# Optimization experiments

Measured on AMD Instinct MI355X. Metric: run time of the kernel, lower is better.

The kernel has to match this reference:

```python
import jax, jax.numpy as jnp
import numpy as np

IMG_C = 256
GC = 32  # graph_channel; must equal graph feature dim 32 for the residual


def setup_inputs() -> dict:
    key = jax.random.key(0)
    ks = jax.random.split(key, 10)
    B, N, WH_SIDE = 8, 4096, 64
    s = lambda fan_in: 1.0 / np.sqrt(fan_in)
    return {
        "input_graph": jax.random.normal(ks[0], (B, N, GC), jnp.float32),
        "input_image": jax.random.normal(ks[1], (B, IMG_C, WH_SIDE, WH_SIDE), jnp.float32),
        # Conv1d(kernel=1) weights stored as [out, in]
        "Wq": jax.random.uniform(ks[2], (GC, 32), jnp.float32, -s(32), s(32)),
        "bq": jax.random.uniform(ks[3], (GC,), jnp.float32, -s(32), s(32)),
        "Wk": jax.random.uniform(ks[4], (GC, IMG_C), jnp.float32, -s(IMG_C), s(IMG_C)),
        "bk": jax.random.uniform(ks[5], (GC,), jnp.float32, -s(IMG_C), s(IMG_C)),
        "Wv": jax.random.uniform(ks[6], (GC, IMG_C), jnp.float32, -s(IMG_C), s(IMG_C)),
        "bv": jax.random.uniform(ks[7], (GC,), jnp.float32, -s(IMG_C), s(IMG_C)),
        "Wc": jax.random.uniform(ks[8], (GC, GC), jnp.float32, -s(GC), s(GC)),
        "bc": jax.random.uniform(ks[9], (GC,), jnp.float32, -s(GC), s(GC)),
    }


def reference(input_graph, input_image, Wq, bq, Wk, bk, Wv, bv, Wc, bc):
    B, C, W, H = input_image.shape
    img = input_image.reshape(B, C, W * H)                      # [B, C, L]
    # 1x1 conv projections == channel matmuls
    K = jnp.einsum('oc,bcl->bol', Wk, img) + bk[None, :, None]  # [B, GC, L]
    V = jnp.einsum('oc,bcl->bol', Wv, img) + bv[None, :, None]  # [B, GC, L]
    # Q: graph [B, N, 32] -> conv over channel dim -> [B, N, GC]
    Q = jnp.einsum('oc,bnc->bno', Wq, input_graph) + bq[None, None, :]
    att = jnp.einsum('bno,bol->bnl', Q, K) / jnp.sqrt(jnp.float32(GC))  # [B, N, L]
    # NOTE: original softmax is over dim=1 (the node/query axis)
    att = jax.nn.softmax(att, axis=1)
    message = jnp.einsum('bol,bnl->bon', V, att)                # [B, GC, N]
    out = input_graph.transpose(0, 2, 1) + (
        jnp.einsum('oc,bcn->bon', Wc, message) + bc[None, :, None]
    )                                                           # [B, GC, N]
    return out.transpose(0, 2, 1)                               # [B, N, GC]
```

## Files before the change

kernel.cpp:

```cpp
#include <hip/hip_runtime.h>

#define BB 8
#define NN 4096
#define LL 4096
#define CC 256

typedef short bf16x8 __attribute__((ext_vector_type(8)));
typedef _Float16 f16x8 __attribute__((ext_vector_type(8)));
typedef _Float16 f16x2 __attribute__((ext_vector_type(2)));
typedef __fp16 hf16x2 __attribute__((ext_vector_type(2)));
typedef float f32x4 __attribute__((ext_vector_type(4)));

__device__ __forceinline__ short f2bf(float f) {
  union { float f; unsigned u; } v; v.f = f;
  unsigned r = v.u + 0x7fffu + ((v.u >> 16) & 1u);
  return (short)(r >> 16);
}
__device__ __forceinline__ bf16x8 ld8(const float* __restrict__ fp) {
  float4 a = *(const float4*)fp;
  float4 b = *(const float4*)(fp + 4);
  bf16x8 r;
  r[0] = f2bf(a.x); r[1] = f2bf(a.y); r[2] = f2bf(a.z); r[3] = f2bf(a.w);
  r[4] = f2bf(b.x); r[5] = f2bf(b.y); r[6] = f2bf(b.z); r[7] = f2bf(b.w);
  return r;
}

__global__ __launch_bounds__(256) void ka_proj(
    const float* __restrict__ graph, const float* __restrict__ img,
    const float* __restrict__ Wq, const float* __restrict__ bq,
    const float* __restrict__ Wk, const float* __restrict__ bk,
    const float* __restrict__ Wv, const float* __restrict__ bv,
    short* __restrict__ Qb, short* __restrict__ Kt, _Float16* __restrict__ Vt)
{
  const int tid = threadIdx.x;
  const int w = tid >> 6, lane = tid & 63, lo = lane & 15, q = lane >> 4;
  const int bid = blockIdx.x;
  if (bid < 512) {
    const int b = bid >> 6;
    const int lt = ((bid & 63) << 6) + (w << 4);
    f32x4 aK0 = {0,0,0,0}, aK1 = {0,0,0,0}, aV0 = {0,0,0,0}, aV1 = {0,0,0,0};
    const float* ib = img + (size_t)b * CC * LL + lt + lo;
    #pragma unroll
    for (int cs = 0; cs < 8; ++cs) {
      const int c0 = cs * 32 + q * 8;
      bf16x8 bi;
      #pragma unroll
      for (int j = 0; j < 8; ++j) bi[j] = f2bf(ib[(size_t)(c0 + j) * LL]);
      bf16x8 wk0 = ld8(Wk + lo * CC + c0);
      bf16x8 wk1 = ld8(Wk + (lo + 16) * CC + c0);
      bf16x8 wv0 = ld8(Wv + lo * CC + c0);
      bf16x8 wv1 = ld8(Wv + (lo + 16) * CC + c0);
      aK0 = __builtin_amdgcn_mfma_f32_16x16x32_bf16(wk0, bi, aK0, 0, 0, 0);
      aK1 = __builtin_amdgcn_mfma_f32_16x16x32_bf16(wk1, bi, aK1, 0, 0, 0);
      aV0 = __builtin_amdgcn_mfma_f32_16x16x32_bf16(wv0, bi, aV0, 0, 0, 0);
      aV1 = __builtin_amdgcn_mfma_f32_16x16x32_bf16(wv1, bi, aV1, 0, 0, 0);
    }
    const float kscale = 0.2550348663f;
    const size_t row = ((size_t)b * LL + lt + lo) * 32;
    short4 s0, s1;
    s0.x = f2bf((aK0[0] + bk[q * 4 + 0]) * kscale);
    s0.y = f2bf((aK0[1] + bk[q * 4 + 1]) * kscale);
    s0.z = f2bf((aK0[2] + bk[q * 4 + 2]) * kscale);
    s0.w = f2bf((aK0[3] + bk[q * 4 + 3]) * kscale);
    s1.x = f2bf((aK1[0] + bk[16 + q * 4 + 0]) * kscale);
    s1.y = f2bf((aK1[1] + bk[16 + q * 4 + 1]) * kscale);
    s1.z = f2bf((aK1[2] + bk[16 + q * 4 + 2]) * kscale);
    s1.w = f2bf((aK1[3] + bk[16 + q * 4 + 3]) * kscale);
    *(short4*)(Kt + row + q * 4) = s0;
    *(short4*)(Kt + row + 16 + q * 4) = s1;
    union { hf16x2 h[2]; uint2 u; } p0, p1;
    p0.h[0] = __builtin_amdgcn_cvt_pkrtz(aV0[0] + bv[q * 4 + 0], aV0[1] + bv[q * 4 + 1]);
    p0.h[1] = __builtin_amdgcn_cvt_pkrtz(aV0[2] + bv[q * 4 + 2], aV0[3] + bv[q * 4 + 3]);
    p1.h[0] = __builtin_amdgcn_cvt_pkrtz(aV1[0] + bv[16 + q * 4 + 0], aV1[1] + bv[16 + q * 4 + 1]);
    p1.h[1] = __builtin_amdgcn_cvt_pkrtz(aV1[2] + bv[16 + q * 4 + 2], aV1[3] + bv[16 + q * 4 + 3]);
    *(uint2*)(Vt + row + q * 4) = p0.u;
    *(uint2*)(Vt + row + 16 + q * 4) = p1.u;
  } else {
    const int t = bid - 512;
    const int b = t >> 6;
    const int nt = ((t & 63) << 6) + (w << 4);
    bf16x8 ag = ld8(graph + ((size_t)b * NN + nt + lo) * 32 + q * 8);
    bf16x8 w0 = ld8(Wq + lo * 32 + q * 8);
    bf16x8 w1 = ld8(Wq + (lo + 16) * 32 + q * 8);
    f32x4 z = {0,0,0,0};
    f32x4 a0 = __builtin_amdgcn_mfma_f32_16x16x32_bf16(ag, w0, z, 0, 0, 0);
    f32x4 a1 = __builtin_amdgcn_mfma_f32_16x16x32_bf16(ag, w1, z, 0, 0, 0);
    const float b0 = bq[lo], b1 = bq[lo + 16];
    #pragma unroll
    for (int r = 0; r < 4; ++r) {
      const size_t rowq = ((size_t)b * NN + nt + q * 4 + r) * 32;
      Qb[rowq + lo] = f2bf(a0[r] + b0);
      Qb[rowq + 16 + lo] = f2bf(a1[r] + b1);
    }
  }
}

__global__ __launch_bounds__(1024) void kb_z(
    const short* __restrict__ Qb, const short* __restrict__ Kt,
    const _Float16* __restrict__ Vt, _Float16* __restrict__ Vpp)
{
  __shared__ float zpart[16][64];
  __shared__ float zinv[64];
  const int tid = threadIdx.x;
  const int w = tid >> 6, lane = tid & 63, lo = lane & 15, q = lane >> 4;
  const int b = blockIdx.x >> 6;
  const int l0 = (blockIdx.x & 63) << 6;
  bf16x8 kf[4];
  #pragma unroll
  for (int f = 0; f < 4; ++f)
    kf[f] = *(const bf16x8*)(Kt + ((size_t)b * LL + l0 + f * 16 + lo) * 32 + q * 8);
  float za[4][4] = {{0}};
  const short* qbase = Qb + ((size_t)b * NN + w * 256 + lo) * 32 + q * 8;
  for (int it = 0; it < 16; ++it) {
    bf16x8 qf = *(const bf16x8*)(qbase + it * 512);
    #pragma unroll
    for (int f = 0; f < 4; ++f) {
      f32x4 z = {0,0,0,0};
      f32x4 c = __builtin_amdgcn_mfma_f32_16x16x32_bf16(kf[f], qf, z, 0, 0, 0);
      #pragma unroll
      for (int r = 0; r < 4; ++r) za[f][r] += __builtin_amdgcn_exp2f(c[r]);
    }
  }
  #pragma unroll
  for (int m = 1; m < 16; m <<= 1)
    #pragma unroll
    for (int f = 0; f < 4; ++f)
      #pragma unroll
      for (int r = 0; r < 4; ++r)
        za[f][r] += __shfl_xor(za[f][r], m, 64);
  if (lo == 0) {
    #pragma unroll
    for (int f = 0; f < 4; ++f)
      #pragma unroll
      for (int r = 0; r < 4; ++r)
        zpart[w][f * 16 + q * 4 + r] = za[f][r];
  }
  __syncthreads();
  if (tid < 64) {
    float z = 0.f;
    #pragma unroll
    for (int t = 0; t < 16; ++t) z += zpart[t][tid];
    zinv[tid] = 4096.0f / z;
  }
  __syncthreads();
  {
    const int l = tid & 63, og = tid >> 6;
    const float inv = zinv[l];
    const f16x2 vv = *(const f16x2*)(Vt + ((size_t)b * LL + l0 + l) * 32 + og * 2);
    Vpp[((size_t)b * 32 + og * 2 + 0) * LL + l0 + l] = (_Float16)((float)vv[0] * inv);
    Vpp[((size_t)b * 32 + og * 2 + 1) * LL + l0 + l] = (_Float16)((float)vv[1] * inv);
  }
}

__global__ __launch_bounds__(256) void kc_attn(
    const short* __restrict__ Qb, const short* __restrict__ Kt,
    const _Float16* __restrict__ Vpp, const float* __restrict__ graph,
    const float* __restrict__ Wc, const float* __restrict__ bc,
    float* __restrict__ out)
{
  __shared__ __align__(16) _Float16 P[4][32][72];
  __shared__ __align__(16) float msgL[4][32][36];
  const int tid = threadIdx.x;
  const int w = tid >> 6, lane = tid & 63, lo = lane & 15, q = lane >> 4;
  const int b = blockIdx.x >> 7;
  const int n0 = (blockIdx.x & 127) << 5;
  const bf16x8 qf0 = *(const bf16x8*)(Qb + ((size_t)b * NN + n0 + lo) * 32 + q * 8);
  const bf16x8 qf1 = *(const bf16x8*)(Qb + ((size_t)b * NN + n0 + 16 + lo) * 32 + q * 8);
  f32x4 m00 = {0,0,0,0}, m01 = {0,0,0,0}, m10 = {0,0,0,0}, m11 = {0,0,0,0};
  const short* ktb = Kt + (size_t)b * LL * 32 + lo * 32 + q * 8;
  const _Float16* vb0 = Vpp + ((size_t)b * 32 + lo) * LL;
  const _Float16* vb1 = vb0 + (size_t)16 * LL;
  for (int lc = w * 16; lc < w * 16 + 16; ++lc) {
    const int lbase = lc * 64;
    #pragma unroll
    for (int f = 0; f < 4; ++f) {
      bf16x8 kf = *(const bf16x8*)(ktb + (size_t)(lbase + f * 16) * 32);
      f32x4 z = {0,0,0,0};
      f32x4 c0 = __builtin_amdgcn_mfma_f32_16x16x32_bf16(kf, qf0, z, 0, 0, 0);
      f32x4 c1 = __builtin_amdgcn_mfma_f32_16x16x32_bf16(kf, qf1, z, 0, 0, 0);
      union { hf16x2 h[2]; uint2 u; } pk0, pk1;
      pk0.h[0] = __builtin_amdgcn_cvt_pkrtz(__builtin_amdgcn_exp2f(c0[0]),
                                            __builtin_amdgcn_exp2f(c0[1]));
      pk0.h[1] = __builtin_amdgcn_cvt_pkrtz(__builtin_amdgcn_exp2f(c0[2]),
                                            __builtin_amdgcn_exp2f(c0[3]));
      pk1.h[0] = __builtin_amdgcn_cvt_pkrtz(__builtin_amdgcn_exp2f(c1[0]),
                                            __builtin_amdgcn_exp2f(c1[1]));
      pk1.h[1] = __builtin_amdgcn_cvt_pkrtz(__builtin_amdgcn_exp2f(c1[2]),
                                            __builtin_amdgcn_exp2f(c1[3]));
      *(uint2*)&P[w][lo][f * 16 + q * 4] = pk0.u;
      *(uint2*)&P[w][16 + lo][f * 16 + q * 4] = pk1.u;
    }
    #pragma unroll
    for (int k = 0; k < 2; ++k) {
      f16x8 pa0 = *(const f16x8*)&P[w][lo][k * 32 + q * 8];
      f16x8 pa1 = *(const f16x8*)&P[w][16 + lo][k * 32 + q * 8];
      f16x8 v0 = *(const f16x8*)(vb0 + lbase + k * 32 + q * 8);
      f16x8 v1 = *(const f16x8*)(vb1 + lbase + k * 32 + q * 8);
      m00 = __builtin_amdgcn_mfma_f32_16x16x32_f16(pa0, v0, m00, 0, 0, 0);
      m01 = __builtin_amdgcn_mfma_f32_16x16x32_f16(pa0, v1, m01, 0, 0, 0);
      m10 = __builtin_amdgcn_mfma_f32_16x16x32_f16(pa1, v0, m10, 0, 0, 0);
      m11 = __builtin_amdgcn_mfma_f32_16x16x32_f16(pa1, v1, m11, 0, 0, 0);
    }
  }
  #pragma unroll
  for (int r = 0; r < 4; ++r) {
    msgL[w][q * 4 + r][lo] = m00[r];
    msgL[w][q * 4 + r][16 + lo] = m01[r];
    msgL[w][16 + q * 4 + r][lo] = m10[r];
    msgL[w][16 + q * 4 + r][16 + lo] = m11[r];
  }
  __syncthreads();
  const int o = lane & 31, nh = lane >> 5;
  float wcr[32];
  #pragma unroll
  for (int c4 = 0; c4 < 8; ++c4) {
    float4 wc4 = *(const float4*)(Wc + o * 32 + c4 * 4);
    wcr[c4 * 4 + 0] = wc4.x * (1.0f / 4096.0f);
    wcr[c4 * 4 + 1] = wc4.y * (1.0f / 4096.0f);
    wcr[c4 * 4 + 2] = wc4.z * (1.0f / 4096.0f);
    wcr[c4 * 4 + 3] = wc4.w * (1.0f / 4096.0f);
  }
  const float bcv = bc[o];
  #pragma unroll
  for (int rr = 0; rr < 4; ++rr) {
    const int nl = w * 8 + nh * 4 + rr;
    f32x4 s = {0,0,0,0};
    #pragma unroll
    for (int cc = 0; cc < 8; ++cc) {
      f32x4 ma = *(const f32x4*)&msgL[0][nl][cc * 4];
      f32x4 mb = *(const f32x4*)&msgL[1][nl][cc * 4];
      f32x4 mc = *(const f32x4*)&msgL[2][nl][cc * 4];
      f32x4 md = *(const f32x4*)&msgL[3][nl][cc * 4];
      f32x4 m4 = ma + mb + mc + md;
      s[0] += wcr[cc * 4 + 0] * m4[0];
      s[1] += wcr[cc * 4 + 1] * m4[1];
      s[2] += wcr[cc * 4 + 2] * m4[2];
      s[3] += wcr[cc * 4 + 3] * m4[3];
    }
    const size_t idx = ((size_t)b * NN + n0 + nl) * 32 + o;
    out[idx] = s[0] + s[1] + s[2] + s[3] + bcv + graph[idx];
  }
}

extern "C" void kernel_launch(void* const* d_in, const int* in_sizes, int n_in,
                              void* d_out, int out_size, void* d_ws, size_t ws_size,
                              hipStream_t stream) {
  const float* graph = (const float*)d_in[0];
  const float* img   = (const float*)d_in[1];
  const float* Wq    = (const float*)d_in[2];
  const float* bq    = (const float*)d_in[3];
  const float* Wk    = (const float*)d_in[4];
  const float* bk    = (const float*)d_in[5];
  const float* Wv    = (const float*)d_in[6];
  const float* bv    = (const float*)d_in[7];
  const float* Wc    = (const float*)d_in[8];
  const float* bc    = (const float*)d_in[9];
  char* ws = (char*)d_ws;
  short*    Qb  = (short*)(ws + 0);
  short*    Kt  = (short*)(ws + 2097152);
  _Float16* Vt  = (_Float16*)(ws + 4194304);
  _Float16* Vpp = (_Float16*)(ws + 6291456);
  ka_proj<<<dim3(1024), dim3(256), 0, stream>>>(graph, img, Wq, bq, Wk, bk, Wv, bv,
                                                Qb, Kt, Vt);
  kb_z<<<dim3(512), dim3(1024), 0, stream>>>(Qb, Kt, Vt, Vpp);
  kc_attn<<<dim3(1024), dim3(256), 0, stream>>>(Qb, Kt, Vpp, graph, Wc, bc,
                                                (float*)d_out);
}
```

Before: 209.2 us.

## Split column-normalizer into atomic partial-sum pass, add K/V prefetch in attention

```diff
diff --git a/kernel.cpp b/kernel.cpp
--- a/kernel.cpp
+++ b/kernel.cpp
@@ -7,7 +7,6 @@
 
 typedef short bf16x8 __attribute__((ext_vector_type(8)));
 typedef _Float16 f16x8 __attribute__((ext_vector_type(8)));
-typedef _Float16 f16x2 __attribute__((ext_vector_type(2)));
 typedef __fp16 hf16x2 __attribute__((ext_vector_type(2)));
 typedef float f32x4 __attribute__((ext_vector_type(4)));
 
@@ -30,13 +29,15 @@
     const float* __restrict__ Wq, const float* __restrict__ bq,
     const float* __restrict__ Wk, const float* __restrict__ bk,
     const float* __restrict__ Wv, const float* __restrict__ bv,
-    short* __restrict__ Qb, short* __restrict__ Kt, _Float16* __restrict__ Vt)
+    short* __restrict__ Qb, short* __restrict__ Kt, _Float16* __restrict__ Vt,
+    float* __restrict__ Zbuf)
 {
   const int tid = threadIdx.x;
   const int w = tid >> 6, lane = tid & 63, lo = lane & 15, q = lane >> 4;
   const int bid = blockIdx.x;
   if (bid < 512) {
     const int b = bid >> 6;
+    if (tid < 64) Zbuf[(size_t)b * LL + ((bid & 63) << 6) + tid] = 0.0f;
     const int lt = ((bid & 63) << 6) + (w << 4);
     f32x4 aK0 = {0,0,0,0}, aK1 = {0,0,0,0}, aV0 = {0,0,0,0}, aV1 = {0,0,0,0};
     const float* ib = img + (size_t)b * CC * LL + lt + lo;
@@ -95,22 +96,23 @@
   }
 }
 
-__global__ __launch_bounds__(1024) void kb_z(
+__global__ __launch_bounds__(256) void kb1_z(
     const short* __restrict__ Qb, const short* __restrict__ Kt,
-    const _Float16* __restrict__ Vt, _Float16* __restrict__ Vpp)
-{
-  __shared__ float zpart[16][64];
-  __shared__ float zinv[64];
+    float* __restrict__ Z)
+{
   const int tid = threadIdx.x;
   const int w = tid >> 6, lane = tid & 63, lo = lane & 15, q = lane >> 4;
-  const int b = blockIdx.x >> 6;
-  const int l0 = (blockIdx.x & 63) << 6;
+  const int bid = blockIdx.x;
+  const int b = bid >> 8;
+  const int l0 = ((bid >> 2) & 63) << 6;
+  const int nq = bid & 3;
   bf16x8 kf[4];
   #pragma unroll
   for (int f = 0; f < 4; ++f)
     kf[f] = *(const bf16x8*)(Kt + ((size_t)b * LL + l0 + f * 16 + lo) * 32 + q * 8);
   float za[4][4] = {{0}};
-  const short* qbase = Qb + ((size_t)b * NN + w * 256 + lo) * 32 + q * 8;
+  const short* qbase = Qb + ((size_t)b * NN + nq * 1024 + w * 256 + lo) * 32 + q * 8;
+  #pragma unroll 4
   for (int it = 0; it < 16; ++it) {
     bf16x8 qf = *(const bf16x8*)(qbase + it * 512);
     #pragma unroll
@@ -133,23 +135,23 @@
     for (int f = 0; f < 4; ++f)
       #pragma unroll
       for (int r = 0; r < 4; ++r)
-        zpart[w][f * 16 + q * 4 + r] = za[f][r];
-  }
-  __syncthreads();
-  if (tid < 64) {
-    float z = 0.f;
-    #pragma unroll
-    for (int t = 0; t < 16; ++t) z += zpart[t][tid];
-    zinv[tid] = 4096.0f / z;
-  }
-  __syncthreads();
-  {
-    const int l = tid & 63, og = tid >> 6;
-    const float inv = zinv[l];
-    const f16x2 vv = *(const f16x2*)(Vt + ((size_t)b * LL + l0 + l) * 32 + og * 2);
-    Vpp[((size_t)b * 32 + og * 2 + 0) * LL + l0 + l] = (_Float16)((float)vv[0] * inv);
-    Vpp[((size_t)b * 32 + og * 2 + 1) * LL + l0 + l] = (_Float16)((float)vv[1] * inv);
-  }
+        atomicAdd(&Z[(size_t)b * LL + l0 + f * 16 + q * 4 + r], za[f][r]);
+  }
+}
+
+__global__ __launch_bounds__(256) void kb2_scale(
+    const _Float16* __restrict__ Vt, const float* __restrict__ Z,
+    _Float16* __restrict__ Vpp)
+{
+  const int tid = threadIdx.x;
+  const int b = blockIdx.x >> 6;
+  const int l = ((blockIdx.x & 63) << 6) + (tid & 63);
+  const int og = tid >> 6;
+  const float inv = __builtin_amdgcn_rcpf(Z[(size_t)b * LL + l]) * 4096.0f;
+  const f16x8 vv = *(const f16x8*)(Vt + ((size_t)b * LL + l) * 32 + og * 8);
+  #pragma unroll
+  for (int j = 0; j < 8; ++j)
+    Vpp[((size_t)b * 32 + og * 8 + j) * LL + l] = (_Float16)((float)vv[j] * inv);
 }
 
 __global__ __launch_bounds__(256) void kc_attn(
@@ -158,26 +160,42 @@
     const float* __restrict__ Wc, const float* __restrict__ bc,
     float* __restrict__ out)
 {
-  __shared__ __align__(16) _Float16 P[4][32][72];
-  __shared__ __align__(16) float msgL[4][32][36];
+  __shared__ __align__(16) unsigned char smem[4 * 32 * 72 * 2];
   const int tid = threadIdx.x;
   const int w = tid >> 6, lane = tid & 63, lo = lane & 15, q = lane >> 4;
   const int b = blockIdx.x >> 7;
   const int n0 = (blockIdx.x & 127) << 5;
+  _Float16* Pw = (_Float16*)smem + w * (32 * 72);
+  float* MS = (float*)smem;
   const bf16x8 qf0 = *(const bf16x8*)(Qb + ((size_t)b * NN + n0 + lo) * 32 + q * 8);
   const bf16x8 qf1 = *(const bf16x8*)(Qb + ((size_t)b * NN + n0 + 16 + lo) * 32 + q * 8);
   f32x4 m00 = {0,0,0,0}, m01 = {0,0,0,0}, m10 = {0,0,0,0}, m11 = {0,0,0,0};
   const short* ktb = Kt + (size_t)b * LL * 32 + lo * 32 + q * 8;
   const _Float16* vb0 = Vpp + ((size_t)b * 32 + lo) * LL;
   const _Float16* vb1 = vb0 + (size_t)16 * LL;
-  for (int lc = w * 16; lc < w * 16 + 16; ++lc) {
+  const int lc0 = w * 16;
+  bf16x8 kfN[4];
+  #pragma unroll
+  for (int f = 0; f < 4; ++f)
+    kfN[f] = *(const bf16x8*)(ktb + (size_t)(lc0 * 64 + f * 16) * 32);
+  for (int lc = lc0; lc < lc0 + 16; ++lc) {
     const int lbase = lc * 64;
+    bf16x8 kfC[4];
+    #pragma unroll
+    for (int f = 0; f < 4; ++f) kfC[f] = kfN[f];
+    f16x8 vA0 = *(const f16x8*)(vb0 + lbase + q * 8);
+    f16x8 vA1 = *(const f16x8*)(vb0 + lbase + 32 + q * 8);
+    f16x8 vB0 = *(const f16x8*)(vb1 + lbase + q * 8);
+    f16x8 vB1 = *(const f16x8*)(vb1 + lbase + 32 + q * 8);
+    const int lcn = (lc + 1 < lc0 + 16) ? lc + 1 : lc;
+    #pragma unroll
+    for (int f = 0; f < 4; ++f)
+      kfN[f] = *(const bf16x8*)(ktb + (size_t)(lcn * 64 + f * 16) * 32);
     #pragma unroll
     for (int f = 0; f < 4; ++f) {
-      bf16x8 kf = *(const bf16x8*)(ktb + (size_t)(lbase + f * 16) * 32);
       f32x4 z = {0,0,0,0};
-      f32x4 c0 = __builtin_amdgcn_mfma_f32_16x16x32_bf16(kf, qf0, z, 0, 0, 0);
-      f32x4 c1 = __builtin_amdgcn_mfma_f32_16x16x32_bf16(kf, qf1, z, 0, 0, 0);
+      f32x4 c0 = __builtin_amdgcn_mfma_f32_16x16x32_bf16(kfC[f], qf0, z, 0, 0, 0);
+      f32x4 c1 = __builtin_amdgcn_mfma_f32_16x16x32_bf16(kfC[f], qf1, z, 0, 0, 0);
       union { hf16x2 h[2]; uint2 u; } pk0, pk1;
       pk0.h[0] = __builtin_amdgcn_cvt_pkrtz(__builtin_amdgcn_exp2f(c0[0]),
                                             __builtin_amdgcn_exp2f(c0[1]));
@@ -187,27 +205,31 @@
                                             __builtin_amdgcn_exp2f(c1[1]));
       pk1.h[1] = __builtin_amdgcn_cvt_pkrtz(__builtin_amdgcn_exp2f(c1[2]),
                                             __builtin_amdgcn_exp2f(c1[3]));
-      *(uint2*)&P[w][lo][f * 16 + q * 4] = pk0.u;
-      *(uint2*)&P[w][16 + lo][f * 16 + q * 4] = pk1.u;
-    }
-    #pragma unroll
-    for (int k = 0; k < 2; ++k) {
-      f16x8 pa0 = *(const f16x8*)&P[w][lo][k * 32 + q * 8];
-      f16x8 pa1 = *(const f16x8*)&P[w][16 + lo][k * 32 + q * 8];
-      f16x8 v0 = *(const f16x8*)(vb0 + lbase + k * 32 + q * 8);
-      f16x8 v1 = *(const f16x8*)(vb1 + lbase + k * 32 + q * 8);
-      m00 = __builtin_amdgcn_mfma_f32_16x16x32_f16(pa0, v0, m00, 0, 0, 0);
-      m01 = __builtin_amdgcn_mfma_f32_16x16x32_f16(pa0, v1, m01, 0, 0, 0);
-      m10 = __builtin_amdgcn_mfma_f32_16x16x32_f16(pa1, v0, m10, 0, 0, 0);
-      m11 = __builtin_amdgcn_mfma_f32_16x16x32_f16(pa1, v1, m11, 0, 0, 0);
-    }
-  }
+      *(uint2*)&Pw[lo * 72 + f * 16 + q * 4] = pk0.u;
+      *(uint2*)&Pw[(16 + lo) * 72 + f * 16 + q * 4] = pk1.u;
+    }
+    {
+      f16x8 pa00 = *(const f16x8*)&Pw[lo * 72 + q * 8];
+      f16x8 pa01 = *(const f16x8*)&Pw[lo * 72 + 32 + q * 8];
+      f16x8 pa10 = *(const f16x8*)&Pw[(16 + lo) * 72 + q * 8];
+      f16x8 pa11 = *(const f16x8*)&Pw[(16 + lo) * 72 + 32 + q * 8];
+      m00 = __builtin_amdgcn_mfma_f32_16x16x32_f16(pa00, vA0, m00, 0, 0, 0);
+      m10 = __builtin_amdgcn_mfma_f32_16x16x32_f16(pa10, vA0, m10, 0, 0, 0);
+      m01 = __builtin_amdgcn_mfma_f32_16x16x32_f16(pa00, vB0, m01, 0, 0, 0);
+      m11 = __builtin_amdgcn_mfma_f32_16x16x32_f16(pa10, vB0, m11, 0, 0, 0);
+      m00 = __builtin_amdgcn_mfma_f32_16x16x32_f16(pa01, vA1, m00, 0, 0, 0);
+      m10 = __builtin_amdgcn_mfma_f32_16x16x32_f16(pa11, vA1, m10, 0, 0, 0);
+      m01 = __builtin_amdgcn_mfma_f32_16x16x32_f16(pa01, vB1, m01, 0, 0, 0);
+      m11 = __builtin_amdgcn_mfma_f32_16x16x32_f16(pa11, vB1, m11, 0, 0, 0);
+    }
+  }
+  float* MSw = MS + w * (32 * 36);
   #pragma unroll
   for (int r = 0; r < 4; ++r) {
-    msgL[w][q * 4 + r][lo] = m00[r];
-    msgL[w][q * 4 + r][16 + lo] = m01[r];
-    msgL[w][16 + q * 4 + r][lo] = m10[r];
-    msgL[w][16 + q * 4 + r][16 + lo] = m11[r];
+    MSw[(q * 4 + r) * 36 + lo] = m00[r];
+    MSw[(q * 4 + r) * 36 + 16 + lo] = m01[r];
+    MSw[(16 + q * 4 + r) * 36 + lo] = m10[r];
+    MSw[(16 + q * 4 + r) * 36 + 16 + lo] = m11[r];
   }
   __syncthreads();
   const int o = lane & 31, nh = lane >> 5;
@@ -227,10 +249,10 @@
     f32x4 s = {0,0,0,0};
     #pragma unroll
     for (int cc = 0; cc < 8; ++cc) {
-      f32x4 ma = *(const f32x4*)&msgL[0][nl][cc * 4];
-      f32x4 mb = *(const f32x4*)&msgL[1][nl][cc * 4];
-      f32x4 mc = *(const f32x4*)&msgL[2][nl][cc * 4];
-      f32x4 md = *(const f32x4*)&msgL[3][nl][cc * 4];
+      f32x4 ma = *(const f32x4*)&MS[0 * 1152 + nl * 36 + cc * 4];
+      f32x4 mb = *(const f32x4*)&MS[1 * 1152 + nl * 36 + cc * 4];
+      f32x4 mc = *(const f32x4*)&MS[2 * 1152 + nl * 36 + cc * 4];
+      f32x4 md = *(const f32x4*)&MS[3 * 1152 + nl * 36 + cc * 4];
       f32x4 m4 = ma + mb + mc + md;
       s[0] += wcr[cc * 4 + 0] * m4[0];
       s[1] += wcr[cc * 4 + 1] * m4[1];
@@ -260,9 +282,11 @@
   short*    Kt  = (short*)(ws + 2097152);
   _Float16* Vt  = (_Float16*)(ws + 4194304);
   _Float16* Vpp = (_Float16*)(ws + 6291456);
+  float*    Zb  = (float*)(ws + 8388608);
   ka_proj<<<dim3(1024), dim3(256), 0, stream>>>(graph, img, Wq, bq, Wk, bk, Wv, bv,
-                                                Qb, Kt, Vt);
-  kb_z<<<dim3(512), dim3(1024), 0, stream>>>(Qb, Kt, Vt, Vpp);
+                                                Qb, Kt, Vt, Zb);
+  kb1_z<<<dim3(2048), dim3(256), 0, stream>>>(Qb, Kt, Zb);
+  kb2_scale<<<dim3(512), dim3(256), 0, stream>>>(Vt, Zb, Vpp);
   kc_attn<<<dim3(1024), dim3(256), 0, stream>>>(Qb, Kt, Vpp, graph, Wc, bc,
                                                 (float*)d_out);
 }
```

Result: faster. 183.1 us (-12.4%).
